# Optimization experiments

Hardware: AMD Instinct MI355X
Metric: run time of the kernel (lower is better)

The kernel has to match this reference:

```python
import jax, jax.numpy as jnp
import numpy as np

BIN_AGG = 2  # binAgg in binFunc

def pair_mean(x):
    # mean over non-overlapping groups of BIN_AGG along last dim, then repeat back
    B, C, H, W = x.shape
    m = x.reshape(B, C, H, W // BIN_AGG, BIN_AGG).mean(axis=-1)  # [B,C,H,W/2]
    return jnp.repeat(m, BIN_AGG, axis=-1)  # [B,C,H,W]

def bin_active(x):
    # binFunc(x, abs_bin=True) * sign(x): per-pair mean of |x| carrying the sign of x
    return pair_mean(jnp.abs(x)) * jnp.sign(x)

def setup_inputs() -> dict:
    key = jax.random.key(0)
    k1, k2, k3 = jax.random.split(key, 3)
    Cin, Cout, K = 256, 256, 3
    x = jax.random.normal(k1, (32, Cin, 56, 56), jnp.float32)
    bound = 1.0 / np.sqrt(Cin * K * K)  # torch Conv2d default init range
    weight = jax.random.uniform(k2, (Cout, Cin, K, K), jnp.float32, -bound, bound)
    bias = jax.random.uniform(k3, (Cout,), jnp.float32, -bound, bound)
    return {"x": x, "weight": weight, "bias": bias}

def reference(x, weight, bias):
    xb = bin_active(x)
    out = jax.lax.conv_general_dilated(
        xb, weight, window_strides=(1, 1), padding=[(1, 1), (1, 1)],
        dimension_numbers=("NCHW", "OIHW", "NCHW"))
    return out + bias[None, :, None, None]
```

## Files before the change

### kernel.cpp

```cpp
#include <hip/hip_runtime.h>
#include <hip/hip_bf16.h>
#include <cstdint>

typedef unsigned short u16;
typedef __attribute__((ext_vector_type(8))) short short8;
typedef __attribute__((ext_vector_type(4))) float f32x4;

#define NB   32
#define CIN  256
#define HH   56
#define WWID 56
#define HP   58
#define WP   58
#define COUT 256
#define NSPAT (NB*HH*WWID)

__device__ __forceinline__ u16 f2bf(float f) {
  uint32_t u = __float_as_uint(f);
  u += 0x7FFFu + ((u >> 16) & 1u);
  return (u16)(u >> 16);
}

__device__ __forceinline__ void gload16(const void* g, void* lds) {
  auto* gp = reinterpret_cast<const __attribute__((address_space(1))) uint32_t*>(
      reinterpret_cast<uintptr_t>(g));
  auto* lp = reinterpret_cast<__attribute__((address_space(3))) uint32_t*>(
      reinterpret_cast<uintptr_t>(lds));
  __builtin_amdgcn_global_load_lds(gp, lp, 16, 0, 0);
}

__global__ __launch_bounds__(256) void prep_x_kernel(const float* __restrict__ x,
                                                     u16* __restrict__ xbp) {
  const int n = blockIdx.x, hp = blockIdx.y, t = threadIdx.x;
  u16* row = xbp + ((size_t)(n*HP + hp))*WP*CIN;
  if (hp == 0 || hp == HP-1) {
    uint32_t* p = (uint32_t*)row;
    for (int i = t; i < WP*CIN/2; i += 256) p[i] = 0;
    return;
  }
  const int h = hp - 1;
  __shared__ u16 lds[HH*CIN];
  if (t < 224) {
    const int f4 = t % 14, c0 = (t / 14) * 16;
    const int sw = f4 & 7;
    #pragma unroll
    for (int ci = 0; ci < 16; ci++) {
      const int c = c0 + ci;
      const float4 v = *(const float4*)(x + (((size_t)n*CIN + c)*HH + h)*WWID + f4*4);
      const float m01 = 0.5f*(fabsf(v.x)+fabsf(v.y));
      const float m23 = 0.5f*(fabsf(v.z)+fabsf(v.w));
      u16 o[4];
      o[0] = f2bf(v.x == 0.f ? 0.f : copysignf(m01, v.x));
      o[1] = f2bf(v.y == 0.f ? 0.f : copysignf(m01, v.y));
      o[2] = f2bf(v.z == 0.f ? 0.f : copysignf(m23, v.z));
      o[3] = f2bf(v.w == 0.f ? 0.f : copysignf(m23, v.w));
      const int cs = ((((c >> 3) ^ sw) & 31) << 3) | (c & 7);
      #pragma unroll
      for (int j = 0; j < 4; j++)
        lds[(f4*4 + j)*CIN + cs] = o[j];
    }
  }
  __syncthreads();
  if (t < 128) ((uint32_t*)row)[t] = 0;
  else ((uint32_t*)(row + (WP-1)*CIN))[t-128] = 0;
  #pragma unroll
  for (int it = 0; it < 7; it++) {
    const int q = it*256 + t;
    const int w = q >> 5, ck = q & 31;
    const short8 v = *(const short8*)&lds[w*CIN + ((ck ^ ((w >> 2) & 7)) << 3)];
    *(short8*)(row + (size_t)(w+1)*CIN + (ck << 3)) = v;
  }
}

__global__ __launch_bounds__(256) void prep_w_kernel(const float* __restrict__ wsrc,
                                                     u16* __restrict__ wr) {
  const int idx = blockIdx.x*256 + threadIdx.x;
  const int co = idx >> 8, ci = idx & 255;
  const float* s = wsrc + (size_t)idx*9;
  #pragma unroll
  for (int p = 0; p < 9; p++)
    wr[((size_t)p*COUT + co)*CIN + ci] = f2bf(s[p]);
}

__global__ __launch_bounds__(256) void conv_kernel(const u16* __restrict__ xbp,
                                                   const u16* __restrict__ wr,
                                                   const float* __restrict__ bias,
                                                   float* __restrict__ out) {
  __shared__ u16 ldsA[2][128*64];
  __shared__ u16 ldsB[2][128*64];
  const int t = threadIdx.x;
  const int wv = t >> 6, l = t & 63;
  const int bid = blockIdx.x;
  const int b9 = (bid & 7)*196 + (bid >> 3);
  const int ntile = b9 & 1, mtile = b9 >> 1;

  const int cs8 = (((l & 7) ^ (l >> 3)) << 3);
  const int rb  = wv*8 + (l >> 3);

  int base0[4];
  #pragma unroll
  for (int i = 0; i < 4; i++) {
    const int m  = mtile*128 + i*32 + rb;
    const int n  = m / 3136, hw = m % 3136;
    base0[i] = ((n*HP + hw/WWID)*WP + (hw%WWID))*CIN;
  }

  auto STAGE = [&](int buf, int ks) {
    const int pos = ks >> 2, cb = ks & 3;
    const int posoff = ((pos/3)*WP + (pos%3))*CIN;
    const int koff = cb*64 + cs8;
    #pragma unroll
    for (int i = 0; i < 4; i++) {
      const u16* gA = wr + (((pos*COUT + ntile*128 + i*32 + rb) << 8) + koff);
      gload16(gA, &ldsA[buf][(i*4 + wv)*512]);
      const u16* gB = xbp + base0[i] + posoff + koff;
      gload16(gB, &ldsB[buf][(i*4 + wv)*512]);
    }
  };

  f32x4 acc[4][4];
  #pragma unroll
  for (int a = 0; a < 4; a++)
    #pragma unroll
    for (int b = 0; b < 4; b++) {
      acc[a][b][0] = 0.f; acc[a][b][1] = 0.f; acc[a][b][2] = 0.f; acc[a][b][3] = 0.f;
    }

  STAGE(0, 0);
  __syncthreads();
  int cur = 0;
  for (int ks = 0; ks < 36; ks++) {
    if (ks < 35) STAGE(cur ^ 1, ks + 1);
    #pragma unroll
    for (int kk = 0; kk < 2; kk++) {
      const int ch = (l >> 4) + 4*kk;
      short8 af[4], bfr[4];
      #pragma unroll
      for (int mi = 0; mi < 4; mi++) {
        const int r = (wv & 1)*64 + mi*16 + (l & 15);
        af[mi] = *(const short8*)&ldsA[cur][r*64 + ((ch ^ (r & 7)) << 3)];
      }
      #pragma unroll
      for (int ni = 0; ni < 4; ni++) {
        const int r = (wv >> 1)*64 + ni*16 + (l & 15);
        bfr[ni] = *(const short8*)&ldsB[cur][r*64 + ((ch ^ (r & 7)) << 3)];
      }
      #pragma unroll
      for (int mi = 0; mi < 4; mi++)
        #pragma unroll
        for (int ni = 0; ni < 4; ni++)
          acc[mi][ni] = __builtin_amdgcn_mfma_f32_16x16x32_bf16(af[mi], bfr[ni], acc[mi][ni], 0, 0, 0);
    }
    __syncthreads();
    cur ^= 1;
  }

  const int co0 = ntile*128 + (wv & 1)*64 + ((l >> 4) << 2);
  float bi[4][4];
  #pragma unroll
  for (int mi = 0; mi < 4; mi++)
    #pragma unroll
    for (int j = 0; j < 4; j++)
      bi[mi][j] = bias[co0 + mi*16 + j];
  const int mb = mtile*128 + (wv >> 1)*64 + (l & 15);
  #pragma unroll
  for (int ni = 0; ni < 4; ni++) {
    const int m = mb + ni*16;
    const int n = m / 3136, hw = m % 3136;
    float* orow = out + (size_t)n*COUT*3136 + hw;
    #pragma unroll
    for (int mi = 0; mi < 4; mi++) {
      #pragma unroll
      for (int j = 0; j < 4; j++)
        orow[(size_t)(co0 + mi*16 + j)*3136] = acc[mi][ni][j] + bi[mi][j];
    }
  }
}

extern "C" void kernel_launch(void* const* d_in, const int* in_sizes, int n_in,
                              void* d_out, int out_size, void* d_ws, size_t ws_size,
                              hipStream_t stream) {
  const float* x      = (const float*)d_in[0];
  const float* weight = (const float*)d_in[1];
  const float* bias   = (const float*)d_in[2];
  float* out = (float*)d_out;

  u16* xbp = (u16*)d_ws;
  u16* wrr = xbp + (size_t)NB*HP*WP*CIN;

  prep_x_kernel<<<dim3(NB, HP), 256, 0, stream>>>(x, xbp);
  prep_w_kernel<<<dim3(256), 256, 0, stream>>>(weight, wrr);
  conv_kernel<<<dim3(NSPAT/128 * 2), 256, 0, stream>>>(xbp, wrr, bias, out);
}
```

Baseline: 334.1 us.

## Triple-buffer conv LDS staging with partial vmcnt waits; vectorize prep_x LDS writes

```diff
diff --git a/kernel.cpp b/kernel.cpp
--- a/kernel.cpp
+++ b/kernel.cpp
@@ -4,6 +4,7 @@
 
 typedef unsigned short u16;
 typedef __attribute__((ext_vector_type(8))) short short8;
+typedef __attribute__((ext_vector_type(8))) unsigned short ushort8;
 typedef __attribute__((ext_vector_type(4))) float f32x4;
 
 #define NB   32
@@ -41,23 +42,33 @@
   const int h = hp - 1;
   __shared__ u16 lds[HH*CIN];
   if (t < 224) {
-    const int f4 = t % 14, c0 = (t / 14) * 16;
+    const int f4 = t % 14, cg = t / 14;
     const int sw = f4 & 7;
     #pragma unroll
-    for (int ci = 0; ci < 16; ci++) {
-      const int c = c0 + ci;
-      const float4 v = *(const float4*)(x + (((size_t)n*CIN + c)*HH + h)*WWID + f4*4);
-      const float m01 = 0.5f*(fabsf(v.x)+fabsf(v.y));
-      const float m23 = 0.5f*(fabsf(v.z)+fabsf(v.w));
-      u16 o[4];
-      o[0] = f2bf(v.x == 0.f ? 0.f : copysignf(m01, v.x));
-      o[1] = f2bf(v.y == 0.f ? 0.f : copysignf(m01, v.y));
-      o[2] = f2bf(v.z == 0.f ? 0.f : copysignf(m23, v.z));
-      o[3] = f2bf(v.w == 0.f ? 0.f : copysignf(m23, v.w));
-      const int cs = ((((c >> 3) ^ sw) & 31) << 3) | (c & 7);
-      #pragma unroll
-      for (int j = 0; j < 4; j++)
-        lds[(f4*4 + j)*CIN + cs] = o[j];
+    for (int it = 0; it < 2; it++) {
+      const int c8 = it*16 + cg;
+      const int c0 = c8 * 8;
+      const float* xc = x + (((size_t)n*CIN + c0)*HH + h)*WWID + f4*4;
+      float4 v[8];
+      #pragma unroll
+      for (int r = 0; r < 8; r++) v[r] = *(const float4*)(xc + (size_t)r*HH*WWID);
+      u16 o[8][4];
+      #pragma unroll
+      for (int r = 0; r < 8; r++) {
+        const float m01 = 0.5f*(fabsf(v[r].x)+fabsf(v[r].y));
+        const float m23 = 0.5f*(fabsf(v[r].z)+fabsf(v[r].w));
+        o[r][0] = f2bf(v[r].x == 0.f ? 0.f : copysignf(m01, v[r].x));
+        o[r][1] = f2bf(v[r].y == 0.f ? 0.f : copysignf(m01, v[r].y));
+        o[r][2] = f2bf(v[r].z == 0.f ? 0.f : copysignf(m23, v[r].z));
+        o[r][3] = f2bf(v[r].w == 0.f ? 0.f : copysignf(m23, v[r].w));
+      }
+      const int cs = (c8 ^ sw) << 3;
+      #pragma unroll
+      for (int j = 0; j < 4; j++) {
+        ushort8 pk = { o[0][j], o[1][j], o[2][j], o[3][j],
+                       o[4][j], o[5][j], o[6][j], o[7][j] };
+        *(ushort8*)&lds[(f4*4 + j)*CIN + cs] = pk;
+      }
     }
   }
   __syncthreads();
@@ -86,8 +97,8 @@
                                                    const u16* __restrict__ wr,
                                                    const float* __restrict__ bias,
                                                    float* __restrict__ out) {
-  __shared__ u16 ldsA[2][128*64];
-  __shared__ u16 ldsB[2][128*64];
+  __shared__ u16 ldsA[3][128*64];
+  __shared__ u16 ldsB[3][128*64];
   const int t = threadIdx.x;
   const int wv = t >> 6, l = t & 63;
   const int bid = blockIdx.x;
@@ -127,10 +138,16 @@
     }
 
   STAGE(0, 0);
-  __syncthreads();
-  int cur = 0;
+  STAGE(1, 1);
+  asm volatile("s_waitcnt vmcnt(8)" ::: "memory");
+  __builtin_amdgcn_sched_barrier(0);
+  __builtin_amdgcn_s_barrier();
+  __builtin_amdgcn_sched_barrier(0);
+
+  int cur = 0, nxt = 2;
+  #pragma unroll 1
   for (int ks = 0; ks < 36; ks++) {
-    if (ks < 35) STAGE(cur ^ 1, ks + 1);
+    if (ks < 34) STAGE(nxt, ks + 2);
     #pragma unroll
     for (int kk = 0; kk < 2; kk++) {
       const int ch = (l >> 4) + 4*kk;
@@ -151,8 +168,15 @@
         for (int ni = 0; ni < 4; ni++)
           acc[mi][ni] = __builtin_amdgcn_mfma_f32_16x16x32_bf16(af[mi], bfr[ni], acc[mi][ni], 0, 0, 0);
     }
-    __syncthreads();
-    cur ^= 1;
+    if (ks < 35) {
+      if (ks < 34) { asm volatile("s_waitcnt vmcnt(8)" ::: "memory"); }
+      else         { asm volatile("s_waitcnt vmcnt(0)" ::: "memory"); }
+      __builtin_amdgcn_sched_barrier(0);
+      __builtin_amdgcn_s_barrier();
+      __builtin_amdgcn_sched_barrier(0);
+    }
+    cur = (cur == 2) ? 0 : cur + 1;
+    nxt = (nxt == 2) ? 0 : nxt + 1;
   }
 
   const int co0 = ntile*128 + (wv & 1)*64 + ((l >> 4) << 2);
```

Result: slower. 374.3 us (+12.0%).
